# Performance work log

Measured on AMD Instinct MI355X. Metric: run time of the kernel, lower is better.

Reference implementation:

```python
import jax, jax.numpy as jnp
import numpy as np

NUM_BASE = 92
NUM_NOVEL = 40
GAMMA = 2.0
ALPHA = 0.25
DISTIL_FACTOR = 1.0
BSZ, N_DET, DIM_FEAT, DIM_HID, DIM_EMB = 16, 48, 2048, 1024, 512
EMB_HALF = DIM_EMB // 2


def _pair_ids(n):
    # all ordered pairs (i, j), i != j  (trajid2pairid)
    s, o = np.meshgrid(np.arange(n), np.arange(n), indexing='ij')
    m = s != o
    return s[m].astype(np.int32), o[m].astype(np.int32)


def _norm(x, eps=1e-12):
    # F.normalize(dim=-1)
    return x / jnp.maximum(jnp.linalg.norm(x, axis=-1, keepdims=True), eps)


def _sigmoid_focal_loss(logits, targets):
    # torchvision.ops.sigmoid_focal_loss, alpha=0.25, gamma=2, reduction='none'
    p = jax.nn.sigmoid(logits)
    ce = jnp.maximum(logits, 0) - logits * targets + jnp.log1p(jnp.exp(-jnp.abs(logits)))
    p_t = p * targets + (1.0 - p) * (1.0 - targets)
    loss = ce * (1.0 - p_t) ** GAMMA
    a_t = ALPHA * targets + (1.0 - ALPHA) * (1.0 - targets)
    return a_t * loss


def setup_inputs() -> dict:
    key = jax.random.key(0)
    ks = jax.random.split(key, 12)
    sids_np, oids_np = _pair_ids(N_DET)
    P = sids_np.shape[0]  # 2256 pairs per video
    w = lambda k, shape, s=0.02: jax.random.normal(k, shape, dtype=jnp.float32) * s
    return {
        'det_feats': jax.random.normal(ks[0], (BSZ, N_DET, DIM_FEAT), dtype=jnp.float32),
        'traj_embds': jax.random.normal(ks[1], (BSZ, N_DET, EMB_HALF), dtype=jnp.float32),
        'relpos_feats': jax.random.normal(ks[2], (BSZ, P, 12), dtype=jnp.float32),
        'classifier_weights': _norm(jax.random.normal(ks[3], (NUM_BASE, DIM_EMB), dtype=jnp.float32)) / np.sqrt(2.0),
        'W1': w(ks[4], (2 * DIM_FEAT, DIM_HID)), 'b1': jnp.zeros((DIM_HID,), jnp.float32),
        'W2': w(ks[5], (DIM_HID, DIM_HID)), 'b2': jnp.zeros((DIM_HID,), jnp.float32),
        'W3': w(ks[6], (DIM_HID, DIM_EMB)),
        'R1': w(ks[7], (12, 256), 0.1), 'rb1': jnp.zeros((256,), jnp.float32),
        'R2': w(ks[8], (256, DIM_EMB), 0.1),
        'temperature': jnp.full((1,), 0.02, dtype=jnp.float32),
        'labels': jax.random.randint(ks[9], (BSZ, P, 1 + NUM_BASE + NUM_NOVEL), 0, 2, dtype=jnp.int32),
        'sids': jnp.asarray(sids_np),
        'oids': jnp.asarray(oids_np),
    }


def reference(det_feats, traj_embds, relpos_feats, classifier_weights,
              W1, b1, W2, b2, W3, R1, rb1, R2, temperature,
              labels, sids, oids):
    Df = det_feats.shape[-1]
    De = traj_embds.shape[-1]
    # gather subject / object features for all pairs, flatten batch
    s_f = det_feats[:, sids, :].reshape(-1, Df)   # [N, Df]
    o_f = det_feats[:, oids, :].reshape(-1, Df)
    so = jnp.concatenate([s_f, o_f], axis=-1)      # [N, 2*Df]
    # trajpair_proj MLP
    h = jax.nn.relu(so @ W1 + b1)
    h = jax.nn.relu(h @ W2 + b2)
    so_proj = h @ W3                                # [N, dim_emb]
    so_n = _norm(so_proj)
    # relpos branch
    rp = relpos_feats.reshape(-1, relpos_feats.shape[-1])
    re = jax.nn.relu(rp @ R1 + rb1) @ R2
    re = _norm(re)
    combined = _norm(so_n + re)
    logits = (combined @ classifier_weights.T) / temperature  # [N, num_base]
    # cls_loss_on_base
    lab = labels.reshape(-1, 1 + NUM_BASE + NUM_NOVEL).astype(logits.dtype)
    pos_mask = jnp.any(lab[:, 1:1 + NUM_BASE] > 0, axis=-1)
    neg_mask = lab[:, 0] > 0
    lab_base = lab[:, 1:1 + NUM_BASE]
    fl_pos = _sigmoid_focal_loss(logits, lab_base)
    pos_den = jnp.maximum(pos_mask.sum(), 1).astype(logits.dtype) * NUM_BASE
    pos_loss = jnp.sum(fl_pos * pos_mask[:, None]) / pos_den
    fl_neg = _sigmoid_focal_loss(logits, jnp.zeros_like(logits))
    neg_den = jnp.maximum(neg_mask.sum(), 1).astype(logits.dtype) * NUM_BASE
    neg_loss = jnp.sum(fl_neg * neg_mask[:, None]) / neg_den
    # distillation L1 loss
    s_e = traj_embds[:, sids, :].reshape(-1, De)
    o_e = traj_embds[:, oids, :].reshape(-1, De)
    distil_target = jnp.concatenate([s_e, o_e], axis=-1)  # [N, dim_emb]
    distil_loss = jnp.mean(jnp.abs(distil_target - so_proj)) * DISTIL_FACTOR
    total_loss = pos_loss + neg_loss + distil_loss
    return total_loss
```

## Files before the change

kernel.cpp:

```cpp
#include <hip/hip_runtime.h>
#include <math.h>

constexpr int BSZ   = 16;
constexpr int NDET  = 48;
constexpr int PAIRS = NDET * (NDET - 1);
constexpr int ROWS  = BSZ * PAIRS;
constexpr int DF    = 2048;
constexpr int DH    = 1024;
constexpr int DE    = 512;
constexpr int EHALF = 256;
constexpr int NCLS  = 92;
constexpr int NPAD  = 128;
constexpr int LABW  = 1 + 92 + 40;

typedef __attribute__((ext_vector_type(8))) short bf16x8;
typedef __attribute__((ext_vector_type(4))) float f32x4;

__device__ __forceinline__ short f2bf(float f) {
    union { float f; unsigned u; } a; a.f = f;
    unsigned r = a.u + 0x7fffu + ((a.u >> 16) & 1u);
    return (short)(r >> 16);
}
__device__ __forceinline__ float bf2f(short h) {
    union { unsigned u; float f; } x;
    x.u = ((unsigned)(unsigned short)h) << 16;
    return x.f;
}

constexpr int N4DET = BSZ * NDET * DF / 4;
constexpr int N4CWT = NPAD * DE / 4;
constexpr int NCONVB = (N4DET + N4CWT) / 256;

struct TransJobs {
    const float* src[5];
    short*       dst[5];
    int K[5], N[5];
    int cum[6];
};

__global__ __launch_bounds__(256) void prep_kernel(
    const float* __restrict__ det, short* __restrict__ det_bf,
    const float* __restrict__ cw, short* __restrict__ cwt, TransJobs jobs)
{
    if (blockIdx.x < NCONVB) {
        int i = blockIdx.x * 256 + threadIdx.x;
        if (i < N4DET) {
            float4 v = ((const float4*)det)[i];
            short4 o;
            o.x = f2bf(v.x); o.y = f2bf(v.y); o.z = f2bf(v.z); o.w = f2bf(v.w);
            ((short4*)det_bf)[i] = o;
        } else {
            int k = i - N4DET;
            int n = (k * 4) >> 9;
            short4 o = {0, 0, 0, 0};
            if (n < NCLS) {
                float4 v = ((const float4*)cw)[k];
                o.x = f2bf(v.x); o.y = f2bf(v.y); o.z = f2bf(v.z); o.w = f2bf(v.w);
            }
            ((short4*)cwt)[k] = o;
        }
        return;
    }
    __shared__ float tile[32][33];
    int t = blockIdx.x - NCONVB;
    int j = 0;
    while (t >= jobs.cum[j + 1]) ++j;
    int lt = t - jobs.cum[j];
    int K = jobs.K[j], N = jobs.N[j];
    int nx = N >> 5;
    int ky = lt / nx, nxi = lt - ky * nx;
    int n0 = nxi * 32, k0 = ky * 32;
    const float* src = jobs.src[j];
    short* dst = jobs.dst[j];
    int tx = threadIdx.x & 31, ty = threadIdx.x >> 5;
#pragma unroll
    for (int i = ty; i < 32; i += 8)
        tile[i][tx] = src[(size_t)(k0 + i) * N + n0 + tx];
    __syncthreads();
#pragma unroll
    for (int i = ty; i < 32; i += 8)
        dst[(size_t)(n0 + i) * K + k0 + tx] = f2bf(tile[tx][i]);
}

__device__ __forceinline__ void load16_lds(const void* g, void* l) {
    __builtin_amdgcn_global_load_lds(
        (const __attribute__((address_space(1))) unsigned int*)g,
        (__attribute__((address_space(3))) unsigned int*)l, 16, 0, 0);
}

template <bool BIAS, bool RELU, bool OUTBF16, bool SWIZZLE, bool DUAL>
__global__ __launch_bounds__(256, 4) void mfma_gemm(
    const short* __restrict__ A, const short* __restrict__ Bt,
    const float* __restrict__ bias, void* __restrict__ C,
    int M, int N, int K, int lda, int ldb,
    const short* A2, const short* Bt2, void* C2, int nsplit,
    int K2, int lda2, int ldb2)
{
    __shared__ __align__(16) char smem_raw[32768];
    short* As = (short*)smem_raw;
    short* Bs = As + 128 * 64;

    int bx, by;
    if (SWIZZLE) {
        int nb  = gridDim.x;
        int gid = blockIdx.y * nb + blockIdx.x;
        int xcd = gid & 7;
        int j   = gid >> 3;
        int rows_per = gridDim.y >> 3;
        int lr  = j / nb;
        bx = j - lr * nb;
        by = xcd * rows_per + lr;
    } else {
        bx = blockIdx.x; by = blockIdx.y;
    }
    if (DUAL && bx >= nsplit) {
        bx -= nsplit; A = A2; Bt = Bt2; C = C2; K = K2; lda = lda2; ldb = ldb2;
    }
    if (by * 128 >= M) return;

    const int tid  = threadIdx.x;
    const int wave = tid >> 6;
    const int lane = tid & 63;
    const int m0 = by * 128;
    const int n0 = bx * 128;
    const int wm = (wave & 1) * 64;
    const int wn = (wave >> 1) * 64;

    f32x4 acc[4][4] = {};

    const int q  = lane >> 4;
    const int lm = lane & 15;

    for (int k0 = 0; k0 < K; k0 += 64) {
#pragma unroll
        for (int it = 0; it < 4; ++it) {
            int c    = (it & 1) * 256 + tid;
            int half = it >> 1;
            int row  = c >> 2;
            int kk   = (c & 3) * 8 + half * 32;
            int ldsc = half * 4096 + ((it & 1) * 256 + wave * 64) * 8;
            int gm = m0 + row; if (gm >= M) gm = M - 1;
            load16_lds(A + (size_t)gm * lda + k0 + kk, As + ldsc);
            int gn = n0 + row;
            load16_lds(Bt + (size_t)gn * ldb + k0 + kk, Bs + ldsc);
        }
        __syncthreads();

#pragma unroll
        for (int half = 0; half < 2; ++half) {
            const short* Ah = As + half * 4096;
            const short* Bh = Bs + half * 4096;
            bf16x8 af[4], bfr[4];
#pragma unroll
            for (int t = 0; t < 4; ++t) {
                af[t]  = *(const bf16x8*)(Ah + (wm + t * 16 + lm) * 32 + q * 8);
                bfr[t] = *(const bf16x8*)(Bh + (wn + t * 16 + lm) * 32 + q * 8);
            }
#pragma unroll
            for (int tm = 0; tm < 4; ++tm)
#pragma unroll
                for (int tn = 0; tn < 4; ++tn)
                    acc[tm][tn] = __builtin_amdgcn_mfma_f32_16x16x32_bf16(
                        af[tm], bfr[tn], acc[tm][tn], 0, 0, 0);
        }
        __syncthreads();
    }

    if (OUTBF16) {
        float* scratch = (float*)smem_raw + wave * (16 * 68);
#pragma unroll
        for (int tm = 0; tm < 4; ++tm) {
            __syncthreads();
#pragma unroll
            for (int tn = 0; tn < 4; ++tn) {
                float bv = BIAS ? bias[n0 + wn + tn * 16 + lm] : 0.0f;
#pragma unroll
                for (int r = 0; r < 4; ++r) {
                    float v = acc[tm][tn][r] + bv;
                    if (RELU) v = fmaxf(v, 0.0f);
                    scratch[(q * 4 + r) * 68 + tn * 16 + lm] = v;
                }
            }
            __syncthreads();
#pragma unroll
            for (int p = 0; p < 2; ++p) {
                int row16 = (lane >> 3) + p * 8;
                int c0 = (lane & 7) * 8;
                float4 v0 = *(float4*)&scratch[row16 * 68 + c0];
                float4 v1 = *(float4*)&scratch[row16 * 68 + c0 + 4];
                bf16x8 o;
                o[0] = f2bf(v0.x); o[1] = f2bf(v0.y); o[2] = f2bf(v0.z); o[3] = f2bf(v0.w);
                o[4] = f2bf(v1.x); o[5] = f2bf(v1.y); o[6] = f2bf(v1.z); o[7] = f2bf(v1.w);
                int grow = m0 + wm + tm * 16 + row16;
                if (grow < M)
                    *(bf16x8*)((short*)C + (size_t)grow * N + n0 + wn + c0) = o;
            }
        }
    } else {
#pragma unroll
        for (int tm = 0; tm < 4; ++tm)
#pragma unroll
            for (int tn = 0; tn < 4; ++tn) {
                int col = n0 + wn + tn * 16 + lm;
#pragma unroll
                for (int r = 0; r < 4; ++r) {
                    int row = m0 + wm + tm * 16 + q * 4 + r;
                    if (row < M) {
                        float v = acc[tm][tn][r];
                        if (BIAS) v += bias[col];
                        if (RELU) v = fmaxf(v, 0.0f);
                        ((float*)C)[(size_t)row * N + col] = v;
                    }
                }
            }
    }
}

constexpr int N4UV = BSZ * NDET * 2048 / 4;
__global__ __launch_bounds__(256) void uvmerge_kernel(
    short* __restrict__ UVa, const short* __restrict__ UVb,
    const float* __restrict__ b1)
{
    int i = blockIdx.x * 256 + threadIdx.x;
    if (i >= N4UV) return;
    short4 a = ((const short4*)UVa)[i];
    short4 b = ((const short4*)UVb)[i];
    int col4 = i & 511;
    float4 bb = {0.0f, 0.0f, 0.0f, 0.0f};
    if (col4 < 256) bb = ((const float4*)b1)[col4];
    short4 o;
    o.x = f2bf(bf2f(a.x) + bf2f(b.x) + bb.x);
    o.y = f2bf(bf2f(a.y) + bf2f(b.y) + bb.y);
    o.z = f2bf(bf2f(a.z) + bf2f(b.z) + bb.z);
    o.w = f2bf(bf2f(a.w) + bf2f(b.w) + bb.w);
    ((short4*)UVa)[i] = o;
}

__global__ __launch_bounds__(256) void pairs_rh_kernel(
    const short* __restrict__ UVs,
    const int* __restrict__ sids, const int* __restrict__ oids,
    short* __restrict__ h1,
    const float* __restrict__ rp, const float* __restrict__ R1,
    const float* __restrict__ rb1, short* __restrict__ rh, int b0)
{
    int r = blockIdx.x;
    int b = b0 + r / PAIRS;
    int p = r % PAIRS;
    int j = threadIdx.x;

    size_t soff = (size_t)(b * NDET + sids[p]) * 2048;
    size_t ooff = (size_t)(b * NDET + oids[p]) * 2048 + 1024;
    short4 a1 = ((const short4*)(UVs + soff))[j];
    short4 a3 = ((const short4*)(UVs + ooff))[j];
    short4 h;
    h.x = f2bf(fmaxf(bf2f(a1.x) + bf2f(a3.x), 0.0f));
    h.y = f2bf(fmaxf(bf2f(a1.y) + bf2f(a3.y), 0.0f));
    h.z = f2bf(fmaxf(bf2f(a1.z) + bf2f(a3.z), 0.0f));
    h.w = f2bf(fmaxf(bf2f(a1.w) + bf2f(a3.w), 0.0f));
    ((short4*)(h1 + (size_t)r * DH))[j] = h;

    int rg = b0 * PAIRS + r;
    const float* row = rp + (size_t)rg * 12;
    float acc = rb1[j];
#pragma unroll
    for (int k = 0; k < 12; ++k) acc = fmaf(row[k], R1[k * 256 + j], acc);
    rh[(size_t)r * 256 + j] = f2bf(fmaxf(acc, 0.0f));
}

__global__ __launch_bounds__(256) void row_prep_kernel(
    const short* __restrict__ sp_bf, const short* __restrict__ ru_bf,
    const float* __restrict__ traj, const float* __restrict__ temperature,
    const int* __restrict__ sids, const int* __restrict__ oids,
    short* __restrict__ comb_bf, float* __restrict__ dist_arr, int b0)
{
    int wave = threadIdx.x >> 6, lane = threadIdx.x & 63;
    int r = blockIdx.x * 4 + wave;
    int rg = b0 * PAIRS + r;
    int b = b0 + r / PAIRS;
    int p = r % PAIRS;

    bf16x8 sv = ((const bf16x8*)(sp_bf + (size_t)r * DE))[lane];
    bf16x8 uv = ((const bf16x8*)(ru_bf + (size_t)r * DE))[lane];
    float s[8], u[8];
#pragma unroll
    for (int i = 0; i < 8; ++i) { s[i] = bf2f(sv[i]); u[i] = bf2f(uv[i]); }

    const float* tsrc = (lane < 32)
        ? (traj + (size_t)(b * NDET + sids[p]) * EHALF + lane * 8)
        : (traj + (size_t)(b * NDET + oids[p]) * EHALF + (lane - 32) * 8);
    float4 t0 = ((const float4*)tsrc)[0], t1 = ((const float4*)tsrc)[1];
    float t[8] = {t0.x, t0.y, t0.z, t0.w, t1.x, t1.y, t1.z, t1.w};

    float ss = 0.0f, sr = 0.0f, sd = 0.0f;
#pragma unroll
    for (int i = 0; i < 8; ++i) {
        ss += s[i] * s[i];
        sr += u[i] * u[i];
        sd += fabsf(t[i] - s[i]);
    }
#pragma unroll
    for (int m = 1; m < 64; m <<= 1) {
        ss += __shfl_xor(ss, m);
        sr += __shfl_xor(sr, m);
        sd += __shfl_xor(sd, m);
    }
    float inv_s = 1.0f / fmaxf(sqrtf(ss), 1e-12f);
    float inv_r = 1.0f / fmaxf(sqrtf(sr), 1e-12f);

    float c[8], sc = 0.0f;
#pragma unroll
    for (int i = 0; i < 8; ++i) {
        c[i] = s[i] * inv_s + u[i] * inv_r;
        sc += c[i] * c[i];
    }
#pragma unroll
    for (int m = 1; m < 64; m <<= 1) sc += __shfl_xor(sc, m);

    float scale = (1.0f / fmaxf(sqrtf(sc), 1e-12f)) / temperature[0];

    bf16x8 o;
#pragma unroll
    for (int i = 0; i < 8; ++i) o[i] = f2bf(c[i] * scale);
    ((bf16x8*)(comb_bf + (size_t)r * DE))[lane] = o;

    if (lane == 0) dist_arr[rg] = sd;
}

__global__ __launch_bounds__(256) void focal_kernel(
    const float* __restrict__ logits, const int* __restrict__ labels,
    float4* __restrict__ pn, int b0)
{
    int wave = threadIdx.x >> 6, lane = threadIdx.x & 63;
    int r = blockIdx.x * 4 + wave;
    int rg = b0 * PAIRS + r;
    const float* lrow = logits + (size_t)r * NPAD;
    size_t labbase = (size_t)rg * LABW;

    float flp = 0.0f, fln = 0.0f, fm = 0.0f;
    for (int c = lane; c < NCLS; c += 64) {
        float l = lrow[c];
        int t = labels[labbase + 1 + c];
        if (t > 0) fm = 1.0f;
        float tf = (float)t;
        float pr = 1.0f / (1.0f + expf(-l));
        float lg = log1pf(expf(-fabsf(l)));
        float ce = fmaxf(l, 0.0f) - l * tf + lg;
        float pt = pr * tf + (1.0f - pr) * (1.0f - tf);
        float om = 1.0f - pt;
        float at = 0.25f * tf + 0.75f * (1.0f - tf);
        flp += at * ce * om * om;
        float ce0 = fmaxf(l, 0.0f) + lg;
        fln += 0.75f * ce0 * pr * pr;
    }
#pragma unroll
    for (int m = 1; m < 64; m <<= 1) {
        flp += __shfl_xor(flp, m);
        fln += __shfl_xor(fln, m);
        fm  += __shfl_xor(fm, m);
    }
    if (lane == 0) {
        int posf = (fm > 0.5f) ? 1 : 0;
        int negf = (labels[labbase] > 0) ? 1 : 0;
        pn[rg] = make_float4(posf ? flp : 0.0f, negf ? fln : 0.0f, 0.0f,
                             (float)(posf + 2 * negf));
    }
}

struct RedRec { double sp, sn, sd; int cp, cn; };
constexpr int RED1 = 64;
constexpr int ROWS_PER_RED = ROWS / RED1;

__global__ __launch_bounds__(256) void reduce1_kernel(
    const float4* __restrict__ pn, const float* __restrict__ dist_arr,
    RedRec* __restrict__ scratch)
{
    int tid = threadIdx.x;
    int base = blockIdx.x * ROWS_PER_RED;
    double sp = 0.0, sn = 0.0, sd = 0.0;
    int cp = 0, cn = 0;
    for (int i = tid; i < ROWS_PER_RED; i += 256) {
        float4 v = pn[base + i];
        sp += (double)v.x; sn += (double)v.y; sd += (double)dist_arr[base + i];
        int f = (int)v.w;
        cp += f & 1; cn += (f >> 1) & 1;
    }
    __shared__ double A[256], B[256], C[256];
    __shared__ int I[256], J[256];
    A[tid] = sp; B[tid] = sn; C[tid] = sd; I[tid] = cp; J[tid] = cn;
    __syncthreads();
    for (int st = 128; st > 0; st >>= 1) {
        if (tid < st) { A[tid] += A[tid + st]; B[tid] += B[tid + st]; C[tid] += C[tid + st];
                        I[tid] += I[tid + st]; J[tid] += J[tid + st]; }
        __syncthreads();
    }
    if (tid == 0) {
        RedRec rec; rec.sp = A[0]; rec.sn = B[0]; rec.sd = C[0];
        rec.cp = I[0]; rec.cn = J[0];
        scratch[blockIdx.x] = rec;
    }
}

__global__ __launch_bounds__(64) void reduce2_kernel(
    const RedRec* __restrict__ scratch, float* __restrict__ out)
{
    int lane = threadIdx.x;
    RedRec rec = scratch[lane];
    double sp = rec.sp, sn = rec.sn, sd = rec.sd;
    int cp = rec.cp, cn = rec.cn;
#pragma unroll
    for (int m = 1; m < 64; m <<= 1) {
        sp += __shfl_xor(sp, m);
        sn += __shfl_xor(sn, m);
        sd += __shfl_xor(sd, m);
        cp += __shfl_xor(cp, m);
        cn += __shfl_xor(cn, m);
    }
    if (lane == 0) {
        int cpv = cp < 1 ? 1 : cp;
        int cnv = cn < 1 ? 1 : cn;
        out[0] = (float)(sp / ((double)cpv * NCLS) +
                         sn / ((double)cnv * NCLS) +
                         sd / ((double)ROWS * DE));
    }
}

static inline int pad8(int x) { return (x + 7) & ~7; }

extern "C" void kernel_launch(void* const* d_in, const int* in_sizes, int n_in,
                              void* d_out, int out_size, void* d_ws, size_t ws_size,
                              hipStream_t stream)
{
    const float* det    = (const float*)d_in[0];
    const float* traj   = (const float*)d_in[1];
    const float* relpos = (const float*)d_in[2];
    const float* cw     = (const float*)d_in[3];
    const float* W1     = (const float*)d_in[4];
    const float* b1     = (const float*)d_in[5];
    const float* W2     = (const float*)d_in[6];
    const float* b2     = (const float*)d_in[7];
    const float* W3     = (const float*)d_in[8];
    const float* R1     = (const float*)d_in[9];
    const float* rb1    = (const float*)d_in[10];
    const float* R2     = (const float*)d_in[11];
    const float* temp   = (const float*)d_in[12];
    const int*   labels = (const int*)d_in[13];
    const int*   sids   = (const int*)d_in[14];
    const int*   oids   = (const int*)d_in[15];
    float* out = (float*)d_out;

    char* ws = (char*)d_ws;
    size_t off = 0;
    auto carve = [&](size_t bytes) -> char* {
        char* p = ws + off;
        off = (off + bytes + 255) & ~(size_t)255;
        return p;
    };
    float4* pn       = (float4*)carve((size_t)ROWS * 16);
    float*  dist_arr = (float*)carve((size_t)ROWS * 4);
    short*  det_bf   = (short*)carve((size_t)BSZ * NDET * DF * 2);
    short*  W1t      = (short*)carve((size_t)2048 * 2048 * 2);
    short*  W2t      = (short*)carve((size_t)DH * DH * 2);
    short*  W3t      = (short*)carve((size_t)DE * DH * 2);
    short*  R2t      = (short*)carve((size_t)DE * 256 * 2);
    short*  cwt      = (short*)carve((size_t)NPAD * DE * 2);
    short*  UVa      = (short*)carve((size_t)BSZ * NDET * 2048 * 2);
    short*  UVb      = (short*)carve((size_t)BSZ * NDET * 2048 * 2);
    size_t fixed_off = off;

    int b_ch = 1;
    for (int cand : {16, 8, 4, 2, 1}) {
        size_t rows  = (size_t)cand * PAIRS;
        size_t bytes = fixed_off + rows * 2048 + 256 + rows * 2048 + 256
                     + rows * 512 + 256 + rows * 1024 + 256;
        if (bytes <= ws_size) { b_ch = cand; break; }
    }
    const int chunk_rows = b_ch * PAIRS;
    const int n_chunks = BSZ / b_ch;
    char* reg1 = carve((size_t)chunk_rows * 2048);
    char* reg2 = carve((size_t)chunk_rows * 2048);
    char* reg3 = carve((size_t)chunk_rows * 512);
    short* comb_bf = (short*)carve((size_t)chunk_rows * 1024);

    short* h1      = (short*)reg1;
    short* h2      = (short*)reg2;
    short* so_bf   = (short*)reg1;
    short* re_bf   = (short*)reg2;
    short* rh      = (short*)reg3;
    float* logits  = (float*)reg3;
    RedRec* red_scratch = (RedRec*)comb_bf;

    TransJobs tj;
    tj.src[0] = W1;                    tj.dst[0] = W1t;                   tj.K[0] = DF;  tj.N[0] = DH;
    tj.src[1] = W1 + (size_t)DF * DH;  tj.dst[1] = W1t + (size_t)DH * DF; tj.K[1] = DF;  tj.N[1] = DH;
    tj.src[2] = W2;                    tj.dst[2] = W2t;                   tj.K[2] = DH;  tj.N[2] = DH;
    tj.src[3] = W3;                    tj.dst[3] = W3t;                   tj.K[3] = DH;  tj.N[3] = DE;
    tj.src[4] = R2;                    tj.dst[4] = R2t;                   tj.K[4] = 256; tj.N[4] = DE;
    tj.cum[0] = 0;
    for (int i = 0; i < 5; ++i)
        tj.cum[i + 1] = tj.cum[i] + (tj.K[i] / 32) * (tj.N[i] / 32);
    prep_kernel<<<NCONVB + tj.cum[5], 256, 0, stream>>>(det, det_bf, cw, cwt, tj);

    mfma_gemm<false, false, true, false, true>
        <<<dim3(32, 6), 256, 0, stream>>>(
        det_bf, W1t, nullptr, UVa, BSZ * NDET, 2048, 1024, 2048, 2048,
        det_bf + 1024, W1t + 1024, UVb, 16, 1024, 2048, 2048);

    uvmerge_kernel<<<(N4UV + 255) / 256, 256, 0, stream>>>(UVa, UVb, b1);

    const int mg  = (chunk_rows + 127) / 128;
    const int mgp = pad8(mg);

    for (int c = 0; c < n_chunks; ++c) {
        int b0 = c * b_ch;
        int r0 = b0 * PAIRS;

        pairs_rh_kernel<<<chunk_rows, 256, 0, stream>>>(
            UVa, sids, oids, h1, relpos, R1, rb1, rh, b0);

        mfma_gemm<true, true, true, true, false>
            <<<dim3(DH / 128, mgp), 256, 0, stream>>>(
            h1, W2t, b2, h2, chunk_rows, DH, DH, DH, DH,
            nullptr, nullptr, nullptr, 0, 0, 0, 0);

        mfma_gemm<false, false, true, true, true>
            <<<dim3(8, mgp), 256, 0, stream>>>(
            h2, W3t, nullptr, so_bf, chunk_rows, DE, DH, DH, DH,
            rh, R2t, re_bf, 4, 256, 256, 256);

        row_prep_kernel<<<chunk_rows / 4, 256, 0, stream>>>(
            so_bf, re_bf, traj, temp, sids, oids, comb_bf, dist_arr, b0);

        mfma_gemm<false, false, false, true, false>
            <<<dim3(1, mgp), 256, 0, stream>>>(
            comb_bf, cwt, nullptr, logits, chunk_rows, NPAD, DE, DE, DE,
            nullptr, nullptr, nullptr, 0, 0, 0, 0);

        focal_kernel<<<chunk_rows / 4, 256, 0, stream>>>(logits, labels, pn, b0);
    }

    reduce1_kernel<<<RED1, 256, 0, stream>>>(pn, dist_arr, red_scratch);
    reduce2_kernel<<<1, 64, 0, stream>>>(red_scratch, out);
}
```

Measured before the change: 393.7 us.

## Fold classifier into W3/R2 projections and fuse row-prep with focal loss

Precomputes W3·cw^T and R2·cw^T once, appending them as 128 extra output columns to the so/re projection GEMMs. Logits are then recovered per row from the raw projections via the norms, and the combined norm comes from ss, sr and the dot product rather than a second reduction. This removes the separate classifier GEMM, the comb_bf round trip and the focal kernel launch per chunk. In exchange the projection GEMMs get wider outputs, and the logits are now formed from bf16-rounded folded weights, which changes rounding behaviour.

```diff
diff --git a/kernel.cpp b/kernel.cpp
--- a/kernel.cpp
+++ b/kernel.cpp
@@ -10,7 +10,7 @@
 constexpr int DE    = 512;
 constexpr int EHALF = 256;
 constexpr int NCLS  = 92;
-constexpr int NPAD  = 128;
+constexpr int NEXT  = DE + 128;
 constexpr int LABW  = 1 + 92 + 40;
 
 typedef __attribute__((ext_vector_type(8))) short bf16x8;
@@ -28,8 +28,10 @@
 }
 
 constexpr int N4DET = BSZ * NDET * DF / 4;
-constexpr int N4CWT = NPAD * DE / 4;
-constexpr int NCONVB = (N4DET + N4CWT) / 256;
+constexpr int N4CWT = 128 * DE / 4;
+constexpr int N4W3  = DH * DE / 4;
+constexpr int N4R2  = 256 * DE / 4;
+constexpr int NCONVB = (N4DET + N4CWT + N4W3 + N4R2) / 256;
 
 struct TransJobs {
     const float* src[5];
@@ -40,17 +42,17 @@
 
 __global__ __launch_bounds__(256) void prep_kernel(
     const float* __restrict__ det, short* __restrict__ det_bf,
-    const float* __restrict__ cw, short* __restrict__ cwt, TransJobs jobs)
+    const float* __restrict__ cw, short* __restrict__ cwt,
+    const float* __restrict__ W3, short* __restrict__ W3bf,
+    const float* __restrict__ R2, short* __restrict__ R2bf,
+    TransJobs jobs)
 {
     if (blockIdx.x < NCONVB) {
         int i = blockIdx.x * 256 + threadIdx.x;
-        if (i < N4DET) {
-            float4 v = ((const float4*)det)[i];
-            short4 o;
-            o.x = f2bf(v.x); o.y = f2bf(v.y); o.z = f2bf(v.z); o.w = f2bf(v.w);
-            ((short4*)det_bf)[i] = o;
-        } else {
-            int k = i - N4DET;
+        const float* src; short* dst; int k;
+        if (i < N4DET) { src = det; dst = det_bf; k = i; }
+        else if (i < N4DET + N4CWT) {
+            k = i - N4DET;
             int n = (k * 4) >> 9;
             short4 o = {0, 0, 0, 0};
             if (n < NCLS) {
@@ -58,7 +60,14 @@
                 o.x = f2bf(v.x); o.y = f2bf(v.y); o.z = f2bf(v.z); o.w = f2bf(v.w);
             }
             ((short4*)cwt)[k] = o;
+            return;
         }
+        else if (i < N4DET + N4CWT + N4W3) { src = W3; dst = W3bf; k = i - N4DET - N4CWT; }
+        else { src = R2; dst = R2bf; k = i - N4DET - N4CWT - N4W3; }
+        float4 v = ((const float4*)src)[k];
+        short4 o;
+        o.x = f2bf(v.x); o.y = f2bf(v.y); o.z = f2bf(v.z); o.w = f2bf(v.w);
+        ((short4*)dst)[k] = o;
         return;
     }
     __shared__ float tile[32][33];
@@ -94,7 +103,7 @@
     const float* __restrict__ bias, void* __restrict__ C,
     int M, int N, int K, int lda, int ldb,
     const short* A2, const short* Bt2, void* C2, int nsplit,
-    int K2, int lda2, int ldb2)
+    int K2, int lda2, int ldb2, int N2)
 {
     __shared__ __align__(16) char smem_raw[32768];
     short* As = (short*)smem_raw;
@@ -114,7 +123,8 @@
         bx = blockIdx.x; by = blockIdx.y;
     }
     if (DUAL && bx >= nsplit) {
-        bx -= nsplit; A = A2; Bt = Bt2; C = C2; K = K2; lda = lda2; ldb = ldb2;
+        bx -= nsplit; A = A2; Bt = Bt2; C = C2;
+        K = K2; lda = lda2; ldb = ldb2; N = N2;
     }
     if (by * 128 >= M) return;
 
@@ -267,11 +277,12 @@
     rh[(size_t)r * 256 + j] = f2bf(fmaxf(acc, 0.0f));
 }
 
-__global__ __launch_bounds__(256) void row_prep_kernel(
-    const short* __restrict__ sp_bf, const short* __restrict__ ru_bf,
+__global__ __launch_bounds__(256) void rowprep_focal_kernel(
+    const short* __restrict__ so_ext, const short* __restrict__ re_ext,
     const float* __restrict__ traj, const float* __restrict__ temperature,
     const int* __restrict__ sids, const int* __restrict__ oids,
-    short* __restrict__ comb_bf, float* __restrict__ dist_arr, int b0)
+    const int* __restrict__ labels,
+    float4* __restrict__ pn, float* __restrict__ dist_arr, int b0)
 {
     int wave = threadIdx.x >> 6, lane = threadIdx.x & 63;
     int r = blockIdx.x * 4 + wave;
@@ -279,8 +290,10 @@
     int b = b0 + r / PAIRS;
     int p = r % PAIRS;
 
-    bf16x8 sv = ((const bf16x8*)(sp_bf + (size_t)r * DE))[lane];
-    bf16x8 uv = ((const bf16x8*)(ru_bf + (size_t)r * DE))[lane];
+    const short* srow = so_ext + (size_t)r * NEXT;
+    const short* rrow = re_ext + (size_t)r * NEXT;
+    bf16x8 sv = *(const bf16x8*)(srow + lane * 8);
+    bf16x8 uv = *(const bf16x8*)(rrow + lane * 8);
     float s[8], u[8];
 #pragma unroll
     for (int i = 0; i < 8; ++i) { s[i] = bf2f(sv[i]); u[i] = bf2f(uv[i]); }
@@ -291,66 +304,46 @@
     float4 t0 = ((const float4*)tsrc)[0], t1 = ((const float4*)tsrc)[1];
     float t[8] = {t0.x, t0.y, t0.z, t0.w, t1.x, t1.y, t1.z, t1.w};
 
-    float ss = 0.0f, sr = 0.0f, sd = 0.0f;
+    float ss = 0.0f, sr = 0.0f, rho = 0.0f, sd = 0.0f;
 #pragma unroll
     for (int i = 0; i < 8; ++i) {
-        ss += s[i] * s[i];
-        sr += u[i] * u[i];
-        sd += fabsf(t[i] - s[i]);
+        ss  += s[i] * s[i];
+        sr  += u[i] * u[i];
+        rho += s[i] * u[i];
+        sd  += fabsf(t[i] - s[i]);
     }
 #pragma unroll
     for (int m = 1; m < 64; m <<= 1) {
-        ss += __shfl_xor(ss, m);
-        sr += __shfl_xor(sr, m);
-        sd += __shfl_xor(sd, m);
+        ss  += __shfl_xor(ss, m);
+        sr  += __shfl_xor(sr, m);
+        rho += __shfl_xor(rho, m);
+        sd  += __shfl_xor(sd, m);
     }
     float inv_s = 1.0f / fmaxf(sqrtf(ss), 1e-12f);
     float inv_r = 1.0f / fmaxf(sqrtf(sr), 1e-12f);
-
-    float c[8], sc = 0.0f;
-#pragma unroll
-    for (int i = 0; i < 8; ++i) {
-        c[i] = s[i] * inv_s + u[i] * inv_r;
-        sc += c[i] * c[i];
-    }
-#pragma unroll
-    for (int m = 1; m < 64; m <<= 1) sc += __shfl_xor(sc, m);
-
-    float scale = (1.0f / fmaxf(sqrtf(sc), 1e-12f)) / temperature[0];
-
-    bf16x8 o;
-#pragma unroll
-    for (int i = 0; i < 8; ++i) o[i] = f2bf(c[i] * scale);
-    ((bf16x8*)(comb_bf + (size_t)r * DE))[lane] = o;
-
-    if (lane == 0) dist_arr[rg] = sd;
-}
-
-__global__ __launch_bounds__(256) void focal_kernel(
-    const float* __restrict__ logits, const int* __restrict__ labels,
-    float4* __restrict__ pn, int b0)
-{
-    int wave = threadIdx.x >> 6, lane = threadIdx.x & 63;
-    int r = blockIdx.x * 4 + wave;
-    int rg = b0 * PAIRS + r;
-    const float* lrow = logits + (size_t)r * NPAD;
+    float ncomb = sqrtf(fmaxf(2.0f + 2.0f * rho * inv_s * inv_r, 0.0f));
+    float scale = 1.0f / (fmaxf(ncomb, 1e-12f) * temperature[0]);
+
+    float flp = 0.0f, fln = 0.0f, fm = 0.0f;
     size_t labbase = (size_t)rg * LABW;
-
-    float flp = 0.0f, fln = 0.0f, fm = 0.0f;
-    for (int c = lane; c < NCLS; c += 64) {
-        float l = lrow[c];
-        int t = labels[labbase + 1 + c];
-        if (t > 0) fm = 1.0f;
-        float tf = (float)t;
-        float pr = 1.0f / (1.0f + expf(-l));
-        float lg = log1pf(expf(-fabsf(l)));
-        float ce = fmaxf(l, 0.0f) - l * tf + lg;
-        float pt = pr * tf + (1.0f - pr) * (1.0f - tf);
-        float om = 1.0f - pt;
-        float at = 0.25f * tf + 0.75f * (1.0f - tf);
-        flp += at * ce * om * om;
-        float ce0 = fmaxf(l, 0.0f) + lg;
-        fln += 0.75f * ce0 * pr * pr;
+#pragma unroll
+    for (int h = 0; h < 2; ++h) {
+        int c = lane + h * 64;
+        if (c < NCLS) {
+            float l = (bf2f(srow[DE + c]) * inv_s + bf2f(rrow[DE + c]) * inv_r) * scale;
+            int tl = labels[labbase + 1 + c];
+            if (tl > 0) fm = 1.0f;
+            float tf = (float)tl;
+            float pr = 1.0f / (1.0f + expf(-l));
+            float lg = log1pf(expf(-fabsf(l)));
+            float ce = fmaxf(l, 0.0f) - l * tf + lg;
+            float pt = pr * tf + (1.0f - pr) * (1.0f - tf);
+            float om = 1.0f - pt;
+            float at = 0.25f * tf + 0.75f * (1.0f - tf);
+            flp += at * ce * om * om;
+            float ce0 = fmaxf(l, 0.0f) + lg;
+            fln += 0.75f * ce0 * pr * pr;
+        }
     }
 #pragma unroll
     for (int m = 1; m < 64; m <<= 1) {
@@ -363,6 +356,7 @@
         int negf = (labels[labbase] > 0) ? 1 : 0;
         pn[rg] = make_float4(posf ? flp : 0.0f, negf ? fln : 0.0f, 0.0f,
                              (float)(posf + 2 * negf));
+        dist_arr[rg] = sd;
     }
 }
 
@@ -460,18 +454,21 @@
     short*  det_bf   = (short*)carve((size_t)BSZ * NDET * DF * 2);
     short*  W1t      = (short*)carve((size_t)2048 * 2048 * 2);
     short*  W2t      = (short*)carve((size_t)DH * DH * 2);
-    short*  W3t      = (short*)carve((size_t)DE * DH * 2);
-    short*  R2t      = (short*)carve((size_t)DE * 256 * 2);
-    short*  cwt      = (short*)carve((size_t)NPAD * DE * 2);
+    short*  W3t      = (short*)carve((size_t)NEXT * DH * 2);
+    short*  R2t      = (short*)carve((size_t)NEXT * 256 * 2);
+    short*  cwt      = (short*)carve((size_t)128 * DE * 2);
+    short*  W3bf     = (short*)carve((size_t)DH * DE * 2);
+    short*  R2bf     = (short*)carve((size_t)256 * DE * 2);
     short*  UVa      = (short*)carve((size_t)BSZ * NDET * 2048 * 2);
     short*  UVb      = (short*)carve((size_t)BSZ * NDET * 2048 * 2);
+    RedRec* red_scratch = (RedRec*)carve((size_t)RED1 * sizeof(RedRec));
     size_t fixed_off = off;
 
     int b_ch = 1;
     for (int cand : {16, 8, 4, 2, 1}) {
         size_t rows  = (size_t)cand * PAIRS;
         size_t bytes = fixed_off + rows * 2048 + 256 + rows * 2048 + 256
-                     + rows * 512 + 256 + rows * 1024 + 256;
+                     + rows * 512 + 256 + rows * 1280 + 256;
         if (bytes <= ws_size) { b_ch = cand; break; }
     }
     const int chunk_rows = b_ch * PAIRS;
@@ -479,15 +476,13 @@
     char* reg1 = carve((size_t)chunk_rows * 2048);
     char* reg2 = carve((size_t)chunk_rows * 2048);
     char* reg3 = carve((size_t)chunk_rows * 512);
-    short* comb_bf = (short*)carve((size_t)chunk_rows * 1024);
-
-    short* h1      = (short*)reg1;
-    short* h2      = (short*)reg2;
-    short* so_bf   = (short*)reg1;
-    short* re_bf   = (short*)reg2;
-    short* rh      = (short*)reg3;
-    float* logits  = (float*)reg3;
-    RedRec* red_scratch = (RedRec*)comb_bf;
+    char* reg4 = carve((size_t)chunk_rows * 1280);
+
+    short* h1     = (short*)reg1;
+    short* h2     = (short*)reg2;
+    short* so_ext = (short*)reg1;
+    short* rh     = (short*)reg3;
+    short* re_ext = (short*)reg4;
 
     TransJobs tj;
     tj.src[0] = W1;                    tj.dst[0] = W1t;                   tj.K[0] = DF;  tj.N[0] = DH;
@@ -498,12 +493,18 @@
     tj.cum[0] = 0;
     for (int i = 0; i < 5; ++i)
         tj.cum[i + 1] = tj.cum[i] + (tj.K[i] / 32) * (tj.N[i] / 32);
-    prep_kernel<<<NCONVB + tj.cum[5], 256, 0, stream>>>(det, det_bf, cw, cwt, tj);
+    prep_kernel<<<NCONVB + tj.cum[5], 256, 0, stream>>>(
+        det, det_bf, cw, cwt, W3, W3bf, R2, R2bf, tj);
+
+    mfma_gemm<false, false, true, false, true>
+        <<<dim3(10, 1), 256, 0, stream>>>(
+        cwt, W3bf, nullptr, W3t + (size_t)512 * DH, 128, 1024, 512, 512, 512,
+        cwt, R2bf, R2t + (size_t)512 * 256, 8, 512, 512, 512, 256);
 
     mfma_gemm<false, false, true, false, true>
         <<<dim3(32, 6), 256, 0, stream>>>(
         det_bf, W1t, nullptr, UVa, BSZ * NDET, 2048, 1024, 2048, 2048,
-        det_bf + 1024, W1t + 1024, UVb, 16, 1024, 2048, 2048);
+        det_bf + 1024, W1t + 1024, UVb, 16, 1024, 2048, 2048, 2048);
 
     uvmerge_kernel<<<(N4UV + 255) / 256, 256, 0, stream>>>(UVa, UVb, b1);
 
@@ -520,22 +521,15 @@
         mfma_gemm<true, true, true, true, false>
             <<<dim3(DH / 128, mgp), 256, 0, stream>>>(
             h1, W2t, b2, h2, chunk_rows, DH, DH, DH, DH,
-            nullptr, nullptr, nullptr, 0, 0, 0, 0);
+            nullptr, nullptr, nullptr, 0, 0, 0, 0, 0);
 
         mfma_gemm<false, false, true, true, true>
-            <<<dim3(8, mgp), 256, 0, stream>>>(
-            h2, W3t, nullptr, so_bf, chunk_rows, DE, DH, DH, DH,
-            rh, R2t, re_bf, 4, 256, 256, 256);
-
-        row_prep_kernel<<<chunk_rows / 4, 256, 0, stream>>>(
-            so_bf, re_bf, traj, temp, sids, oids, comb_bf, dist_arr, b0);
-
-        mfma_gemm<false, false, false, true, false>
-            <<<dim3(1, mgp), 256, 0, stream>>>(
-            comb_bf, cwt, nullptr, logits, chunk_rows, NPAD, DE, DE, DE,
-            nullptr, nullptr, nullptr, 0, 0, 0, 0);
-
-        focal_kernel<<<chunk_rows / 4, 256, 0, stream>>>(logits, labels, pn, b0);
+            <<<dim3(10, mgp), 256, 0, stream>>>(
+            h2, W3t, nullptr, so_ext, chunk_rows, NEXT, DH, DH, DH,
+            rh, R2t, re_ext, 5, 256, 256, 256, NEXT);
+
+        rowprep_focal_kernel<<<chunk_rows / 4, 256, 0, stream>>>(
+            so_ext, re_ext, traj, temp, sids, oids, labels, pn, dist_arr, b0);
     }
 
     reduce1_kernel<<<RED1, 256, 0, stream>>>(pn, dist_arr, red_scratch);
```

After: 388.4 us. About the same (-1.4%).
